# Performance work log

Hardware: AMD Instinct MI355X
Metric: run time of the kernel (lower is better)

Reference implementation:

```python
import jax, jax.numpy as jnp
import numpy as np

N_NODES = 100000
N_EDGES = 1600000
N_GRAPHS = 256
EPS = 1e-5  # GraphNorm / BatchNorm eps


def _seg_sum(x, seg, n):
    return jax.ops.segment_sum(x, seg, num_segments=n)


def setup_inputs() -> dict:
    key = jax.random.key(0)
    ks = jax.random.split(key, 24)
    f32 = jnp.float32

    def nrm(k, shape, s=0.05):
        return jax.random.normal(k, shape, f32) * s

    inp = {}
    inp["x"] = jax.random.normal(ks[0], (N_NODES, 64), f32)
    inp["edge_attr"] = jax.random.normal(ks[1], (N_EDGES, 8), f32)
    # edge_mlp: Linear(8,16) -> ReLU -> Linear(16,1); final bias +2 keeps degrees positive
    inp["em_w1"] = nrm(ks[2], (16, 8), 0.1); inp["em_b1"] = jnp.zeros((16,), f32)
    inp["em_w2"] = nrm(ks[3], (1, 16), 0.1); inp["em_b2"] = jnp.full((1,), 2.0, f32)
    # GCNConv weights stored (in, out); PyG GCNConv lin has no bias, separate bias after aggregation
    inp["conv_w0"] = nrm(ks[4], (64, 128)); inp["conv_b0"] = jnp.zeros((128,), f32)
    inp["conv_w1"] = nrm(ks[5], (128, 128)); inp["conv_b1"] = jnp.zeros((128,), f32)
    inp["conv_w2"] = nrm(ks[6], (128, 128)); inp["conv_b2"] = jnp.zeros((128,), f32)
    # GraphNorm params: weight=1, bias=0, mean_scale=1 (PyG init)
    for i in range(3):
        inp[f"gn_w{i}"] = jnp.ones((128,), f32)
        inp[f"gn_b{i}"] = jnp.zeros((128,), f32)
        inp[f"gn_ms{i}"] = jnp.ones((128,), f32)
    # MLP head (weights stored (in,out)); BatchNorm1d eval: running_mean=0, running_var=1
    inp["lin_w0"] = nrm(ks[7], (128, 256)); inp["lin_b0"] = jnp.zeros((256,), f32)
    inp["bn_g0"] = jnp.ones((256,), f32); inp["bn_b0"] = jnp.zeros((256,), f32)
    inp["lin_w1"] = nrm(ks[8], (256, 128)); inp["lin_b1"] = jnp.zeros((128,), f32)
    inp["bn_g1"] = jnp.ones((128,), f32); inp["bn_b1"] = jnp.zeros((128,), f32)
    inp["out_w"] = nrm(ks[9], (128, 1)); inp["out_b"] = jnp.zeros((1,), f32)
    inp["edge_index"] = jax.random.randint(ks[10], (2, N_EDGES), 0, N_NODES)
    inp["batch"] = jnp.sort(jax.random.randint(ks[11], (N_NODES,), 0, N_GRAPHS))
    return inp


def _gcn_conv(h, W, b, src, tgt, ew):
    # PyG GCNConv with edge_weight: add self-loops (weight 1), symmetric normalization
    hw = h @ W  # [N, out]
    deg = _seg_sum(ew, tgt, N_NODES) + 1.0  # in-degree incl. self-loop
    dinv = jnp.where(deg > 0, jax.lax.rsqrt(deg), 0.0)
    norm_e = dinv[src] * ew * dinv[tgt]  # [E]
    agg = _seg_sum(norm_e[:, None] * hw[src], tgt, N_NODES)
    agg = agg + (dinv * dinv)[:, None] * hw  # self-loop contribution
    return agg + b


def _graph_norm(h, batch, w, b, ms, cnt):
    mean = _seg_sum(h, batch, N_GRAPHS) / cnt[:, None]  # [G, C]
    sub = h - ms * mean[batch]
    var = _seg_sum(sub * sub, batch, N_GRAPHS) / cnt[:, None]
    return w * sub / jnp.sqrt(var + EPS)[batch] + b


def reference(x, edge_attr, em_w1, em_b1, em_w2, em_b2,
              conv_w0, conv_b0, conv_w1, conv_b1, conv_w2, conv_b2,
              gn_w0, gn_b0, gn_ms0, gn_w1, gn_b1, gn_ms1, gn_w2, gn_b2, gn_ms2,
              lin_w0, lin_b0, bn_g0, bn_b0, lin_w1, lin_b1, bn_g1, bn_b1,
              out_w, out_b, edge_index, batch):
    src, tgt = edge_index[0], edge_index[1]
    ew = (jax.nn.relu(edge_attr @ em_w1.T + em_b1) @ em_w2.T + em_b2).reshape(-1)  # [E]
    cnt = jnp.maximum(_seg_sum(jnp.ones((N_NODES,), x.dtype), batch, N_GRAPHS), 1.0)

    h = x
    layers = [(conv_w0, conv_b0, gn_w0, gn_b0, gn_ms0),
              (conv_w1, conv_b1, gn_w1, gn_b1, gn_ms1),
              (conv_w2, conv_b2, gn_w2, gn_b2, gn_ms2)]
    for W, b, gw, gb, gms in layers:
        h = _gcn_conv(h, W, b, src, tgt, ew)
        h = _graph_norm(h, batch, gw, gb, gms, cnt)
        h = jax.nn.relu(h)  # dropout is identity in eval mode

    pooled = _seg_sum(h, batch, N_GRAPHS) / cnt[:, None]  # global_mean_pool [G, 128]

    inv = 1.0 / jnp.sqrt(1.0 + EPS)  # BatchNorm1d eval: mean=0, var=1
    h = jax.nn.relu((pooled @ lin_w0 + lin_b0) * inv * bn_g0 + bn_b0)
    h = jax.nn.relu((h @ lin_w1 + lin_b1) * inv * bn_g1 + bn_b1)
    out = h @ out_w + out_b  # [G, 1]
    return (out, h)
```

## Files before the change

### kernel.cpp

```cpp
#include <hip/hip_runtime.h>

#define N_NODES 100000
#define N_EDGES 1600000
#define N_GRAPHS 256
#define EPS 1e-5f

#define SCAN_BLOCKS ((N_NODES + 255) / 256)

typedef __attribute__((ext_vector_type(8))) short bfrag8;
typedef __attribute__((ext_vector_type(4))) float facc4;

__device__ __forceinline__ void fma4(float4& a, float s, const float4& w) {
  a.x += s * w.x; a.y += s * w.y; a.z += s * w.z; a.w += s * w.w;
}

__device__ __forceinline__ unsigned short f2bf(float f) {
  union { float f; unsigned u; } x;
  x.f = f;
  unsigned r = x.u + 0x7FFF + ((x.u >> 16) & 1);
  return (unsigned short)(r >> 16);
}
__device__ __forceinline__ unsigned packbf(float a, float b) {
  return (unsigned)f2bf(a) | ((unsigned)f2bf(b) << 16);
}
__device__ __forceinline__ float4 bf4(uint2 v) {
  union { unsigned u; float f; } a, b, c, d;
  a.u = v.x << 16;
  b.u = v.x & 0xFFFF0000u;
  c.u = v.y << 16;
  d.u = v.y & 0xFFFF0000u;
  return make_float4(a.f, b.f, c.f, d.f);
}

__global__ __launch_bounds__(256) void k_edge_mlp(
    const float* __restrict__ ea, const float* __restrict__ w1,
    const float* __restrict__ b1, const float* __restrict__ w2,
    const float* __restrict__ b2, const int* __restrict__ tgt,
    float* __restrict__ ew, int* __restrict__ rowcnt,
    int* __restrict__ rank) {
  __shared__ float W1[128], B1[16], W2[16];
  int t = threadIdx.x;
  if (t < 128) W1[t] = w1[t];
  if (t < 16) { B1[t] = b1[t]; W2[t] = w2[t]; }
  __syncthreads();
  int e = blockIdx.x * 256 + t;
  if (e >= N_EDGES) return;
  const float4* ap = (const float4*)(ea + (size_t)e * 8);
  float4 a0 = ap[0], a1 = ap[1];
  float a[8] = {a0.x, a0.y, a0.z, a0.w, a1.x, a1.y, a1.z, a1.w};
  float out = b2[0];
#pragma unroll
  for (int i = 0; i < 16; ++i) {
    float h = B1[i];
#pragma unroll
    for (int j = 0; j < 8; ++j) h += a[j] * W1[i * 8 + j];
    out += fmaxf(h, 0.f) * W2[i];
  }
  ew[e] = out;
  rank[e] = atomicAdd(&rowcnt[tgt[e]], 1);
}

__global__ __launch_bounds__(256) void k_cvt(const float* __restrict__ x,
                                             unsigned* __restrict__ xb) {
  int i = blockIdx.x * 256 + threadIdx.x;
  if (i >= N_NODES * 64 / 8) return;
  const float4* p = (const float4*)(x + (size_t)i * 8);
  float4 a = p[0], b = p[1];
  uint4 o;
  o.x = packbf(a.x, a.y);
  o.y = packbf(a.z, a.w);
  o.z = packbf(b.x, b.y);
  o.w = packbf(b.z, b.w);
  ((uint4*)xb)[i] = o;
}

__global__ __launch_bounds__(256) void k_cvtw(
    const float* __restrict__ w1, const float* __restrict__ w2,
    unsigned short* __restrict__ o1, unsigned short* __restrict__ o2) {
  int id = blockIdx.x * 256 + threadIdx.x;
  const float* w = blockIdx.y ? w2 : w1;
  unsigned short* o = blockIdx.y ? o2 : o1;
  int n = id >> 7, k = id & 127;
  o[n * 128 + k] = f2bf(w[k * 128 + n]);
}

__global__ __launch_bounds__(256) void k_scan1(const int* __restrict__ cnt,
                                               int* __restrict__ bsum) {
  int i = blockIdx.x * 256 + threadIdx.x;
  int v = (i < N_NODES) ? cnt[i] : 0;
#pragma unroll
  for (int off = 32; off; off >>= 1) v += __shfl_down(v, off);
  __shared__ int ws[4];
  if ((threadIdx.x & 63) == 0) ws[threadIdx.x >> 6] = v;
  __syncthreads();
  if (threadIdx.x == 0) bsum[blockIdx.x] = ws[0] + ws[1] + ws[2] + ws[3];
}

__global__ __launch_bounds__(512) void k_scan2(const int* __restrict__ bsum,
                                               int* __restrict__ boff) {
  __shared__ int s[512];
  int t = threadIdx.x;
  s[t] = (t < SCAN_BLOCKS) ? bsum[t] : 0;
  __syncthreads();
  for (int off = 1; off < 512; off <<= 1) {
    int u = (t >= off) ? s[t - off] : 0;
    __syncthreads();
    s[t] += u;
    __syncthreads();
  }
  boff[t] = (t == 0) ? 0 : s[t - 1];
}

__global__ __launch_bounds__(256) void k_scan3(const int* __restrict__ cnt,
                                               const int* __restrict__ boff,
                                               int* __restrict__ rowstart) {
  __shared__ int s[256];
  int t = threadIdx.x;
  int i = blockIdx.x * 256 + t;
  int v = (i < N_NODES) ? cnt[i] : 0;
  s[t] = v;
  __syncthreads();
  for (int off = 1; off < 256; off <<= 1) {
    int u = (t >= off) ? s[t - off] : 0;
    __syncthreads();
    s[t] += u;
    __syncthreads();
  }
  if (i < N_NODES) {
    int pre = boff[blockIdx.x] + s[t] - v;
    rowstart[i] = pre;
    if (i == N_NODES - 1) rowstart[N_NODES] = pre + v;
  }
}

__global__ __launch_bounds__(256) void k_fill(
    const int* __restrict__ src, const int* __restrict__ tgt,
    const float* __restrict__ ew, const int* __restrict__ rank,
    const int* __restrict__ rowstart, int* __restrict__ src_s,
    float* __restrict__ ew_s) {
  int e = blockIdx.x * 256 + threadIdx.x;
  if (e >= N_EDGES) return;
  int p = rowstart[tgt[e]] + rank[e];
  src_s[p] = src[e];
  ew_s[p] = ew[e];
}

__global__ __launch_bounds__(256) void k_deg(const float* __restrict__ ew_s,
                                             const int* __restrict__ rowstart,
                                             float* __restrict__ dinv) {
  int n = blockIdx.x * 256 + threadIdx.x;
  if (n >= N_NODES) return;
  int rs = rowstart[n], re = rowstart[n + 1];
  float d = 1.f;
  for (int j = rs; j < re; ++j) d += ew_s[j];
  dinv[n] = d > 0.f ? rsqrtf(d) : 0.f;
}

__global__ __launch_bounds__(256) void k_scale(float* __restrict__ ew_s,
                                               const int* __restrict__ src_s,
                                               const int* __restrict__ rowstart,
                                               const float* __restrict__ dinv) {
  int n = blockIdx.x * 4 + (threadIdx.x >> 6);
  if (n >= N_NODES) return;
  int lane = threadIdx.x & 63;
  int rs = rowstart[n], re = rowstart[n + 1];
  float dv = dinv[n];
  for (int j = rs + lane; j < re; j += 64) ew_s[j] *= dinv[src_s[j]] * dv;
}

__global__ void k_starts(const int* __restrict__ batch, int* __restrict__ start) {
  int g = blockIdx.x * blockDim.x + threadIdx.x;
  if (g > N_GRAPHS) return;
  int lo = 0, hi = N_NODES;
  while (lo < hi) {
    int mid = (lo + hi) >> 1;
    if (batch[mid] < g) lo = mid + 1; else hi = mid;
  }
  start[g] = lo;
}

__global__ __launch_bounds__(256) void k_gather64b(
    const unsigned* __restrict__ xb, const float* __restrict__ ew_s,
    const int* __restrict__ src_s, const int* __restrict__ rowstart,
    const float* __restrict__ dinv, float* __restrict__ out) {
  const int t = threadIdx.x;
  const int n = blockIdx.x * 4 + (t >> 6);
  if (n >= N_NODES) return;
  const int lane = t & 63;
  const int q = lane >> 4;
  const int cl = lane & 15;
  const int rs = rowstart[n], re = rowstart[n + 1];
  const uint2* x2 = (const uint2*)xb;
  float4 a0 = make_float4(0.f, 0.f, 0.f, 0.f);
  float4 a1 = make_float4(0.f, 0.f, 0.f, 0.f);
  int j = rs;
  for (; j + 8 <= re; j += 8) {
    int i0 = j + q, i1 = j + 4 + q;
    float w0 = ew_s[i0], w1 = ew_s[i1];
    float4 v0 = bf4(x2[(size_t)src_s[i0] * 16 + cl]);
    float4 v1 = bf4(x2[(size_t)src_s[i1] * 16 + cl]);
    fma4(a0, w0, v0);
    fma4(a1, w1, v1);
  }
  for (; j + 4 <= re; j += 4) {
    int i0 = j + q;
    fma4(a0, ew_s[i0], bf4(x2[(size_t)src_s[i0] * 16 + cl]));
  }
  if (j + q < re) {
    fma4(a1, ew_s[j + q], bf4(x2[(size_t)src_s[j + q] * 16 + cl]));
  }
  a0.x += a1.x; a0.y += a1.y; a0.z += a1.z; a0.w += a1.w;
#pragma unroll
  for (int m = 16; m <= 32; m <<= 1) {
    a0.x += __shfl_xor(a0.x, m);
    a0.y += __shfl_xor(a0.y, m);
    a0.z += __shfl_xor(a0.z, m);
    a0.w += __shfl_xor(a0.w, m);
  }
  if (q == 0) {
    float dv = dinv[n];
    float4 hv = bf4(x2[(size_t)n * 16 + cl]);
    float4 r = make_float4(a0.x + dv * dv * hv.x, a0.y + dv * dv * hv.y,
                           a0.z + dv * dv * hv.z, a0.w + dv * dv * hv.w);
    ((float4*)out)[(size_t)n * 16 + cl] = r;
  }
}

template <int CIN>
__global__ __launch_bounds__(256) void k_hw0(
    const float* __restrict__ h, const float* __restrict__ W,
    const float* __restrict__ bias, float* __restrict__ hw) {
  constexpr int KT = 32;
  __shared__ float hs[64][36];
  __shared__ float Ws[KT][128];
  const int t = threadIdx.x;
  const int tn = t & 15, tc = t >> 4;
  const int base = blockIdx.x * 64;

  float acc[4][8];
#pragma unroll
  for (int i = 0; i < 4; ++i)
#pragma unroll
    for (int j = 0; j < 8; ++j) acc[i][j] = 0.f;

  const int ln = t >> 2;
  const int lk = (t & 3) * 8;
  const int wk = t >> 3;
  const int wc = (t & 7) * 16;

  for (int k0 = 0; k0 < CIN; k0 += KT) {
    __syncthreads();
    {
      int n = base + ln;
      float4 v0 = make_float4(0.f, 0.f, 0.f, 0.f), v1 = v0;
      if (n < N_NODES) {
        const float4* hp = (const float4*)(h + (size_t)n * CIN + k0 + lk);
        v0 = hp[0];
        v1 = hp[1];
      }
      *(float4*)&hs[ln][lk] = v0;
      *(float4*)&hs[ln][lk + 4] = v1;
      const float4* wp = (const float4*)(W + (size_t)(k0 + wk) * 128 + wc);
#pragma unroll
      for (int q = 0; q < 4; ++q) *(float4*)&Ws[wk][wc + q * 4] = wp[q];
    }
    __syncthreads();
#pragma unroll
    for (int kk = 0; kk < KT; kk += 4) {
      float4 hv[4];
#pragma unroll
      for (int i = 0; i < 4; ++i) hv[i] = *(const float4*)&hs[tn + 16 * i][kk];
#pragma unroll
      for (int dk = 0; dk < 4; ++dk) {
        float4 wa = *(const float4*)&Ws[kk + dk][tc * 4];
        float4 wb = *(const float4*)&Ws[kk + dk][64 + tc * 4];
#pragma unroll
        for (int i = 0; i < 4; ++i) {
          float hvv = (&hv[i].x)[dk];
          acc[i][0] += hvv * wa.x; acc[i][1] += hvv * wa.y;
          acc[i][2] += hvv * wa.z; acc[i][3] += hvv * wa.w;
          acc[i][4] += hvv * wb.x; acc[i][5] += hvv * wb.y;
          acc[i][6] += hvv * wb.z; acc[i][7] += hvv * wb.w;
        }
      }
    }
  }
  float4 b_lo = *(const float4*)&bias[tc * 4];
  float4 b_hi = *(const float4*)&bias[64 + tc * 4];
#pragma unroll
  for (int i = 0; i < 4; ++i) {
    int n = base + tn + 16 * i;
    if (n < N_NODES) {
      float* op = hw + (size_t)n * 128;
      *(float4*)&op[tc * 4] =
          make_float4(acc[i][0] + b_lo.x, acc[i][1] + b_lo.y,
                      acc[i][2] + b_lo.z, acc[i][3] + b_lo.w);
      *(float4*)&op[64 + tc * 4] =
          make_float4(acc[i][4] + b_hi.x, acc[i][5] + b_hi.y,
                      acc[i][6] + b_hi.z, acc[i][7] + b_hi.w);
    }
  }
}

__global__ __launch_bounds__(256) void k_hw_mfma(
    const float* __restrict__ h, const unsigned short* __restrict__ wt,
    const int* __restrict__ batch, const float* __restrict__ An,
    const float* __restrict__ Bn, unsigned short* __restrict__ hwb) {
  __shared__ unsigned short Asb[64][136];
  __shared__ unsigned short Wsb[128][136];
  const int t = threadIdx.x;
  const int base = blockIdx.x * 64;

  for (int i = t; i < 2048; i += 256) {
    int nr = i >> 4, k8 = (i & 15) * 8;
    *(uint4*)&Wsb[nr][k8] = *(const uint4*)&wt[nr * 128 + k8];
  }
  {
    const int ln = t >> 2;
    const int cg = (t & 3) * 32;
    const int n = base + ln;
    if (n < N_NODES) {
      const int g = batch[n];
      const float* hp = h + (size_t)n * 128;
      const float* Ap = An + (size_t)g * 128;
      const float* Bp = Bn + (size_t)g * 128;
#pragma unroll
      for (int c4 = 0; c4 < 8; ++c4) {
        int c = cg + c4 * 4;
        float4 v = *(const float4*)&hp[c];
        float4 Af = *(const float4*)&Ap[c];
        float4 Bf = *(const float4*)&Bp[c];
        uint2 o;
        o.x = packbf(fmaxf(Af.x * v.x + Bf.x, 0.f),
                     fmaxf(Af.y * v.y + Bf.y, 0.f));
        o.y = packbf(fmaxf(Af.z * v.z + Bf.z, 0.f),
                     fmaxf(Af.w * v.w + Bf.w, 0.f));
        *(uint2*)&Asb[ln][c] = o;
      }
    } else {
#pragma unroll
      for (int c4 = 0; c4 < 8; ++c4) {
        uint2 o;
        o.x = 0; o.y = 0;
        *(uint2*)&Asb[ln][cg + c4 * 4] = o;
      }
    }
  }
  __syncthreads();

  const int wv = t >> 6;
  const int lr = t & 15;
  const int lk = (t >> 4) & 3;
  const int m0 = wv * 16;

  bfrag8 af[4];
#pragma unroll
  for (int kc = 0; kc < 4; ++kc)
    af[kc] = *(const bfrag8*)&Asb[m0 + lr][kc * 32 + lk * 8];

#pragma unroll
  for (int nt = 0; nt < 8; ++nt) {
    facc4 c = {0.f, 0.f, 0.f, 0.f};
#pragma unroll
    for (int kc = 0; kc < 4; ++kc) {
      bfrag8 bf = *(const bfrag8*)&Wsb[nt * 16 + lr][kc * 32 + lk * 8];
      c = __builtin_amdgcn_mfma_f32_16x16x32_bf16(af[kc], bf, c, 0, 0, 0);
    }
    int col = nt * 16 + lr;
#pragma unroll
    for (int r = 0; r < 4; ++r) {
      int n = base + m0 + lk * 4 + r;
      if (n < N_NODES) hwb[(size_t)n * 128 + col] = f2bf(c[r]);
    }
  }
}

__global__ __launch_bounds__(256) void k_gatherb(
    const unsigned* __restrict__ hwb, const float* __restrict__ ew_s,
    const int* __restrict__ src_s, const int* __restrict__ rowstart,
    const float* __restrict__ dinv, const float* __restrict__ bias,
    float* __restrict__ agg) {
  const int t = threadIdx.x;
  const int n = blockIdx.x * 4 + (t >> 6);
  if (n >= N_NODES) return;
  const int lane = t & 63;
  const int q = lane >> 5;
  const int cl = lane & 31;
  const int rs = rowstart[n], re = rowstart[n + 1];
  const uint2* hb = (const uint2*)hwb;
  float4 a0 = make_float4(0.f, 0.f, 0.f, 0.f);
  float4 a1 = make_float4(0.f, 0.f, 0.f, 0.f);
  float4 a2 = make_float4(0.f, 0.f, 0.f, 0.f);
  float4 a3 = make_float4(0.f, 0.f, 0.f, 0.f);
  int j = rs;
  for (; j + 8 <= re; j += 8) {
    int i0 = j + q, i1 = j + 2 + q, i2 = j + 4 + q, i3 = j + 6 + q;
    float w0 = ew_s[i0], w1 = ew_s[i1], w2 = ew_s[i2], w3 = ew_s[i3];
    float4 v0 = bf4(hb[(size_t)src_s[i0] * 32 + cl]);
    float4 v1 = bf4(hb[(size_t)src_s[i1] * 32 + cl]);
    float4 v2 = bf4(hb[(size_t)src_s[i2] * 32 + cl]);
    float4 v3 = bf4(hb[(size_t)src_s[i3] * 32 + cl]);
    fma4(a0, w0, v0);
    fma4(a1, w1, v1);
    fma4(a2, w2, v2);
    fma4(a3, w3, v3);
  }
  for (; j + 2 <= re; j += 2) {
    int i0 = j + q;
    fma4(a0, ew_s[i0], bf4(hb[(size_t)src_s[i0] * 32 + cl]));
  }
  if (q == 0 && j < re) {
    fma4(a1, ew_s[j], bf4(hb[(size_t)src_s[j] * 32 + cl]));
  }
  a0.x += a1.x + a2.x + a3.x;
  a0.y += a1.y + a2.y + a3.y;
  a0.z += a1.z + a2.z + a3.z;
  a0.w += a1.w + a2.w + a3.w;
  a0.x += __shfl_xor(a0.x, 32);
  a0.y += __shfl_xor(a0.y, 32);
  a0.z += __shfl_xor(a0.z, 32);
  a0.w += __shfl_xor(a0.w, 32);
  if (q == 0) {
    float dv = dinv[n];
    float4 hv = bf4(hb[(size_t)n * 32 + cl]);
    float4 bv = ((const float4*)bias)[cl];
    float4 r = make_float4(a0.x + dv * dv * hv.x + bv.x,
                           a0.y + dv * dv * hv.y + bv.y,
                           a0.z + dv * dv * hv.z + bv.z,
                           a0.w + dv * dv * hv.w + bv.w);
    ((float4*)agg)[(size_t)n * 32 + cl] = r;
  }
}

__global__ __launch_bounds__(512) void k_gstats(
    const float* __restrict__ h, const int* __restrict__ start,
    const float* __restrict__ gw, const float* __restrict__ gb,
    const float* __restrict__ gms, float* __restrict__ An,
    float* __restrict__ Bn) {
  int g = blockIdx.x;
  int s = start[g], e = start[g + 1];
  int t = threadIdx.x, p = t >> 7, c = t & 127;
  float sum = 0.f, sq = 0.f;
  for (int n = s + p; n < e; n += 4) {
    float v = h[(size_t)n * 128 + c];
    sum += v;
    sq += v * v;
  }
  __shared__ float S[4][128], Q[4][128];
  S[p][c] = sum;
  Q[p][c] = sq;
  __syncthreads();
  if (t < 128) {
    float cnt = (float)max(e - s, 1);
    float mean = (S[0][t] + S[1][t] + S[2][t] + S[3][t]) / cnt;
    float e2 = (Q[0][t] + Q[1][t] + Q[2][t] + Q[3][t]) / cnt;
    float ms = gms[t];
    float var = fmaxf(e2 - ms * (2.f - ms) * mean * mean, 0.f);
    float scale = gw[t] / sqrtf(var + EPS);
    An[(size_t)g * 128 + t] = scale;
    Bn[(size_t)g * 128 + t] = gb[t] - scale * ms * mean;
  }
}

__global__ __launch_bounds__(512) void k_pool(
    const float* __restrict__ h, const int* __restrict__ start,
    const float* __restrict__ An, const float* __restrict__ Bn,
    float* __restrict__ pooled) {
  int g = blockIdx.x;
  int s = start[g], e = start[g + 1];
  int t = threadIdx.x, p = t >> 7, c = t & 127;
  float A = An[(size_t)g * 128 + c], B = Bn[(size_t)g * 128 + c];
  float sum = 0.f;
  for (int n = s + p; n < e; n += 4)
    sum += fmaxf(A * h[(size_t)n * 128 + c] + B, 0.f);
  __shared__ float S[4][128];
  S[p][c] = sum;
  __syncthreads();
  if (t < 128) {
    float cnt = (float)max(e - s, 1);
    pooled[g * 128 + t] = (S[0][t] + S[1][t] + S[2][t] + S[3][t]) / cnt;
  }
}

__global__ __launch_bounds__(256) void k_head(
    const float* __restrict__ pooled, const float* __restrict__ w0,
    const float* __restrict__ b0, const float* __restrict__ g0,
    const float* __restrict__ bb0, const float* __restrict__ w1,
    const float* __restrict__ b1, const float* __restrict__ g1,
    const float* __restrict__ bb1, const float* __restrict__ ow,
    const float* __restrict__ ob, float* __restrict__ out) {
  __shared__ float p[128], h1[256], h2[128];
  int g = blockIdx.x, t = threadIdx.x;
  const float inv = 1.0f / sqrtf(1.0f + EPS);
  if (t < 128) p[t] = pooled[g * 128 + t];
  __syncthreads();
  {
    float acc = b0[t];
#pragma unroll 8
    for (int k = 0; k < 128; ++k) acc += p[k] * w0[k * 256 + t];
    h1[t] = fmaxf(acc * inv * g0[t] + bb0[t], 0.f);
  }
  __syncthreads();
  if (t < 128) {
    float acc = b1[t];
#pragma unroll 8
    for (int k = 0; k < 256; ++k) acc += h1[k] * w1[k * 128 + t];
    float v = fmaxf(acc * inv * g1[t] + bb1[t], 0.f);
    h2[t] = v;
    out[N_GRAPHS + g * 128 + t] = v;
  }
  __syncthreads();
  if (t < 64) {
    float v = h2[t] * ow[t] + h2[t + 64] * ow[t + 64];
#pragma unroll
    for (int off = 32; off; off >>= 1) v += __shfl_down(v, off);
    if (t == 0) out[g] = v + ob[0];
  }
}

extern "C" void kernel_launch(void* const* d_in, const int* in_sizes, int n_in,
                              void* d_out, int out_size, void* d_ws,
                              size_t ws_size, hipStream_t stream) {
  const float* x = (const float*)d_in[0];
  const float* edge_attr = (const float*)d_in[1];
  const float* em_w1 = (const float*)d_in[2];
  const float* em_b1 = (const float*)d_in[3];
  const float* em_w2 = (const float*)d_in[4];
  const float* em_b2 = (const float*)d_in[5];
  const float* conv_w[3] = {(const float*)d_in[6], (const float*)d_in[8],
                            (const float*)d_in[10]};
  const float* conv_b[3] = {(const float*)d_in[7], (const float*)d_in[9],
                            (const float*)d_in[11]};
  const float* gn_w[3] = {(const float*)d_in[12], (const float*)d_in[15],
                          (const float*)d_in[18]};
  const float* gn_b[3] = {(const float*)d_in[13], (const float*)d_in[16],
                          (const float*)d_in[19]};
  const float* gn_ms[3] = {(const float*)d_in[14], (const float*)d_in[17],
                           (const float*)d_in[20]};
  const float* lin_w0 = (const float*)d_in[21];
  const float* lin_b0 = (const float*)d_in[22];
  const float* bn_g0 = (const float*)d_in[23];
  const float* bn_b0 = (const float*)d_in[24];
  const float* lin_w1 = (const float*)d_in[25];
  const float* lin_b1 = (const float*)d_in[26];
  const float* bn_g1 = (const float*)d_in[27];
  const float* bn_b1 = (const float*)d_in[28];
  const float* out_w = (const float*)d_in[29];
  const float* out_b = (const float*)d_in[30];
  const int* edge_index = (const int*)d_in[31];
  const int* batch = (const int*)d_in[32];
  const int* src = edge_index;
  const int* tgt = edge_index + N_EDGES;

  char* w = (char*)d_ws;
  size_t off = 0;
  auto carve = [&](size_t bytes) {
    void* p = w + off;
    off = (off + bytes + 511) & ~(size_t)511;
    return p;
  };
  float* ew = (float*)carve((size_t)N_EDGES * 4);
  int* rank = (int*)carve((size_t)N_EDGES * 4);
  float* dinv = (float*)carve((size_t)N_NODES * 4);
  int* rowcnt = (int*)carve((size_t)N_NODES * 4);
  int* rowstart = (int*)carve((size_t)(N_NODES + 1) * 4);
  int* bsum = (int*)carve((size_t)SCAN_BLOCKS * 4);
  int* boff = (int*)carve((size_t)512 * 4);
  int* src_s = (int*)carve((size_t)N_EDGES * 4);
  float* ew_s = (float*)carve((size_t)N_EDGES * 4);
  int* start = (int*)carve((N_GRAPHS + 1) * 4);
  float* AB = (float*)carve((size_t)6 * N_GRAPHS * 128 * 4);
  unsigned* xb = (unsigned*)carve((size_t)N_NODES * 64 * 2);
  unsigned* hwb = (unsigned*)carve((size_t)N_NODES * 128 * 2);
  unsigned short* wt1 = (unsigned short*)carve((size_t)128 * 128 * 2);
  unsigned short* wt2 = (unsigned short*)carve((size_t)128 * 128 * 2);
  float* big1 = (float*)carve((size_t)N_NODES * 128 * 4);
  float* big2 = (float*)carve((size_t)N_NODES * 128 * 4);
  float* pooled = (float*)carve((size_t)N_GRAPHS * 128 * 4);

  float* A0 = AB, *B0 = AB + N_GRAPHS * 128;
  float* A1 = AB + 2 * N_GRAPHS * 128, *B1 = AB + 3 * N_GRAPHS * 128;
  float* A2 = AB + 4 * N_GRAPHS * 128, *B2 = AB + 5 * N_GRAPHS * 128;

  hipMemsetAsync(rowcnt, 0, (size_t)N_NODES * 4, stream);

  k_edge_mlp<<<(N_EDGES + 255) / 256, 256, 0, stream>>>(
      edge_attr, em_w1, em_b1, em_w2, em_b2, tgt, ew, rowcnt, rank);
  k_cvt<<<(N_NODES * 64 / 8 + 255) / 256, 256, 0, stream>>>(x, xb);
  k_cvtw<<<dim3(64, 2), 256, 0, stream>>>(conv_w[1], conv_w[2], wt1, wt2);
  k_scan1<<<SCAN_BLOCKS, 256, 0, stream>>>(rowcnt, bsum);
  k_scan2<<<1, 512, 0, stream>>>(bsum, boff);
  k_scan3<<<SCAN_BLOCKS, 256, 0, stream>>>(rowcnt, boff, rowstart);
  k_fill<<<(N_EDGES + 255) / 256, 256, 0, stream>>>(src, tgt, ew, rank,
                                                    rowstart, src_s, ew_s);
  k_deg<<<(N_NODES + 255) / 256, 256, 0, stream>>>(ew_s, rowstart, dinv);
  k_scale<<<(N_NODES + 3) / 4, 256, 0, stream>>>(ew_s, src_s, rowstart, dinv);
  k_starts<<<1, 512, 0, stream>>>(batch, start);

  const int ggrid = (N_NODES + 3) / 4;
  const int hwgrid = (N_NODES + 63) / 64;

  k_gather64b<<<ggrid, 256, 0, stream>>>(xb, ew_s, src_s, rowstart, dinv,
                                         big2);
  k_hw0<64><<<hwgrid, 256, 0, stream>>>(big2, conv_w[0], conv_b[0], big1);
  k_gstats<<<N_GRAPHS, 512, 0, stream>>>(big1, start, gn_w[0], gn_b[0],
                                         gn_ms[0], A0, B0);
  k_hw_mfma<<<hwgrid, 256, 0, stream>>>(big1, wt1, batch, A0, B0,
                                        (unsigned short*)hwb);
  k_gatherb<<<ggrid, 256, 0, stream>>>(hwb, ew_s, src_s, rowstart, dinv,
                                       conv_b[1], big2);
  k_gstats<<<N_GRAPHS, 512, 0, stream>>>(big2, start, gn_w[1], gn_b[1],
                                         gn_ms[1], A1, B1);
  k_hw_mfma<<<hwgrid, 256, 0, stream>>>(big2, wt2, batch, A1, B1,
                                        (unsigned short*)hwb);
  k_gatherb<<<ggrid, 256, 0, stream>>>(hwb, ew_s, src_s, rowstart, dinv,
                                       conv_b[2], big1);
  k_gstats<<<N_GRAPHS, 512, 0, stream>>>(big1, start, gn_w[2], gn_b[2],
                                         gn_ms[2], A2, B2);

  k_pool<<<N_GRAPHS, 512, 0, stream>>>(big1, start, A2, B2, pooled);
  k_head<<<N_GRAPHS, 256, 0, stream>>>(pooled, lin_w0, lin_b0, bn_g0, bn_b0,
                                       lin_w1, lin_b1, bn_g1, bn_b1, out_w,
                                       out_b, (float*)d_out);
}
```

Before: 594.2 us.

## Store intermediates in bf16, pack edge metadata, use MFMA for first layer

Interleaves source index and edge weight into a single uint2 metadata array so each gather reads one 8-byte record instead of two separate arrays. All node-level intermediates (aggregated features, layer outputs) are now stored as bf16 instead of fp32, halving the traffic of the gstats, pool and hw kernels. The first-layer FP32 tiled GEMM is replaced by a bf16 MFMA kernel with pre-transposed bf16 weights. This cuts memory bandwidth but adds bf16 rounding at more points, which may affect accuracy.

```diff
diff --git a/kernel.cpp b/kernel.cpp
--- a/kernel.cpp
+++ b/kernel.cpp
@@ -23,13 +23,19 @@
 __device__ __forceinline__ unsigned packbf(float a, float b) {
   return (unsigned)f2bf(a) | ((unsigned)f2bf(b) << 16);
 }
-__device__ __forceinline__ float4 bf4(uint2 v) {
+__device__ __forceinline__ float4 bf4(unsigned lo, unsigned hi) {
   union { unsigned u; float f; } a, b, c, d;
-  a.u = v.x << 16;
-  b.u = v.x & 0xFFFF0000u;
-  c.u = v.y << 16;
-  d.u = v.y & 0xFFFF0000u;
+  a.u = lo << 16;
+  b.u = lo & 0xFFFF0000u;
+  c.u = hi << 16;
+  d.u = hi & 0xFFFF0000u;
   return make_float4(a.f, b.f, c.f, d.f);
+}
+__device__ __forceinline__ float bfat(const unsigned* tb, int idx) {
+  unsigned u = tb[idx >> 1];
+  union { unsigned u; float f; } v;
+  v.u = (idx & 1) ? (u & 0xFFFF0000u) : (u << 16);
+  return v.f;
 }
 
 __global__ __launch_bounds__(256) void k_edge_mlp(
@@ -84,6 +90,14 @@
   o[n * 128 + k] = f2bf(w[k * 128 + n]);
 }
 
+__global__ __launch_bounds__(256) void k_cvtw0(const float* __restrict__ w0,
+                                               unsigned short* __restrict__ o) {
+  int id = blockIdx.x * 256 + threadIdx.x;
+  if (id >= 8192) return;
+  int n = id >> 6, k = id & 63;
+  o[n * 64 + k] = f2bf(w0[k * 128 + n]);
+}
+
 __global__ __launch_bounds__(256) void k_scan1(const int* __restrict__ cnt,
                                                int* __restrict__ bsum) {
   int i = blockIdx.x * 256 + threadIdx.x;
@@ -136,28 +150,31 @@
 __global__ __launch_bounds__(256) void k_fill(
     const int* __restrict__ src, const int* __restrict__ tgt,
     const float* __restrict__ ew, const int* __restrict__ rank,
-    const int* __restrict__ rowstart, int* __restrict__ src_s,
-    float* __restrict__ ew_s) {
+    const int* __restrict__ rowstart, uint2* __restrict__ meta) {
   int e = blockIdx.x * 256 + threadIdx.x;
   if (e >= N_EDGES) return;
   int p = rowstart[tgt[e]] + rank[e];
-  src_s[p] = src[e];
-  ew_s[p] = ew[e];
-}
-
-__global__ __launch_bounds__(256) void k_deg(const float* __restrict__ ew_s,
+  union { float f; unsigned u; } w;
+  w.f = ew[e];
+  meta[p] = make_uint2(w.u, (unsigned)src[e]);
+}
+
+__global__ __launch_bounds__(256) void k_deg(const uint2* __restrict__ meta,
                                              const int* __restrict__ rowstart,
                                              float* __restrict__ dinv) {
   int n = blockIdx.x * 256 + threadIdx.x;
   if (n >= N_NODES) return;
   int rs = rowstart[n], re = rowstart[n + 1];
   float d = 1.f;
-  for (int j = rs; j < re; ++j) d += ew_s[j];
+  for (int j = rs; j < re; ++j) {
+    union { unsigned u; float f; } w;
+    w.u = meta[j].x;
+    d += w.f;
+  }
   dinv[n] = d > 0.f ? rsqrtf(d) : 0.f;
 }
 
-__global__ __launch_bounds__(256) void k_scale(float* __restrict__ ew_s,
-                                               const int* __restrict__ src_s,
+__global__ __launch_bounds__(256) void k_scale(uint2* __restrict__ meta,
                                                const int* __restrict__ rowstart,
                                                const float* __restrict__ dinv) {
   int n = blockIdx.x * 4 + (threadIdx.x >> 6);
@@ -165,7 +182,13 @@
   int lane = threadIdx.x & 63;
   int rs = rowstart[n], re = rowstart[n + 1];
   float dv = dinv[n];
-  for (int j = rs + lane; j < re; j += 64) ew_s[j] *= dinv[src_s[j]] * dv;
+  for (int j = rs + lane; j < re; j += 64) {
+    uint2 m = meta[j];
+    union { unsigned u; float f; } w;
+    w.u = m.x;
+    w.f *= dinv[m.y] * dv;
+    meta[j].x = w.u;
+  }
 }
 
 __global__ void k_starts(const int* __restrict__ batch, int* __restrict__ start) {
@@ -180,9 +203,9 @@
 }
 
 __global__ __launch_bounds__(256) void k_gather64b(
-    const unsigned* __restrict__ xb, const float* __restrict__ ew_s,
-    const int* __restrict__ src_s, const int* __restrict__ rowstart,
-    const float* __restrict__ dinv, float* __restrict__ out) {
+    const unsigned* __restrict__ xb, const uint2* __restrict__ meta,
+    const int* __restrict__ rowstart, const float* __restrict__ dinv,
+    unsigned* __restrict__ aggxb) {
   const int t = threadIdx.x;
   const int n = blockIdx.x * 4 + (t >> 6);
   if (n >= N_NODES) return;
@@ -195,19 +218,27 @@
   float4 a1 = make_float4(0.f, 0.f, 0.f, 0.f);
   int j = rs;
   for (; j + 8 <= re; j += 8) {
-    int i0 = j + q, i1 = j + 4 + q;
-    float w0 = ew_s[i0], w1 = ew_s[i1];
-    float4 v0 = bf4(x2[(size_t)src_s[i0] * 16 + cl]);
-    float4 v1 = bf4(x2[(size_t)src_s[i1] * 16 + cl]);
-    fma4(a0, w0, v0);
-    fma4(a1, w1, v1);
+    uint2 m0 = meta[j + q], m1 = meta[j + 4 + q];
+    union { unsigned u; float f; } w0, w1;
+    w0.u = m0.x; w1.u = m1.x;
+    uint2 v0 = x2[(size_t)m0.y * 16 + cl];
+    uint2 v1 = x2[(size_t)m1.y * 16 + cl];
+    fma4(a0, w0.f, bf4(v0.x, v0.y));
+    fma4(a1, w1.f, bf4(v1.x, v1.y));
   }
   for (; j + 4 <= re; j += 4) {
-    int i0 = j + q;
-    fma4(a0, ew_s[i0], bf4(x2[(size_t)src_s[i0] * 16 + cl]));
+    uint2 m0 = meta[j + q];
+    union { unsigned u; float f; } w0;
+    w0.u = m0.x;
+    uint2 v0 = x2[(size_t)m0.y * 16 + cl];
+    fma4(a0, w0.f, bf4(v0.x, v0.y));
   }
   if (j + q < re) {
-    fma4(a1, ew_s[j + q], bf4(x2[(size_t)src_s[j + q] * 16 + cl]));
+    uint2 m0 = meta[j + q];
+    union { unsigned u; float f; } w0;
+    w0.u = m0.x;
+    uint2 v0 = x2[(size_t)m0.y * 16 + cl];
+    fma4(a1, w0.f, bf4(v0.x, v0.y));
   }
   a0.x += a1.x; a0.y += a1.y; a0.z += a1.z; a0.w += a1.w;
 #pragma unroll
@@ -219,91 +250,73 @@
   }
   if (q == 0) {
     float dv = dinv[n];
-    float4 hv = bf4(x2[(size_t)n * 16 + cl]);
-    float4 r = make_float4(a0.x + dv * dv * hv.x, a0.y + dv * dv * hv.y,
-                           a0.z + dv * dv * hv.z, a0.w + dv * dv * hv.w);
-    ((float4*)out)[(size_t)n * 16 + cl] = r;
-  }
-}
-
-template <int CIN>
-__global__ __launch_bounds__(256) void k_hw0(
-    const float* __restrict__ h, const float* __restrict__ W,
-    const float* __restrict__ bias, float* __restrict__ hw) {
-  constexpr int KT = 32;
-  __shared__ float hs[64][36];
-  __shared__ float Ws[KT][128];
+    uint2 hvb = x2[(size_t)n * 16 + cl];
+    float4 hv = bf4(hvb.x, hvb.y);
+    uint2 o;
+    o.x = packbf(a0.x + dv * dv * hv.x, a0.y + dv * dv * hv.y);
+    o.y = packbf(a0.z + dv * dv * hv.z, a0.w + dv * dv * hv.w);
+    *(uint2*)&aggxb[(size_t)n * 32 + cl * 2] = o;
+  }
+}
+
+__global__ __launch_bounds__(256) void k_hw_mfma0(
+    const unsigned short* __restrict__ aggxb,
+    const unsigned short* __restrict__ wt0, const float* __restrict__ bias,
+    unsigned short* __restrict__ h1b) {
+  __shared__ unsigned short Asb[64][72];
+  __shared__ unsigned short Wsb[128][72];
   const int t = threadIdx.x;
-  const int tn = t & 15, tc = t >> 4;
   const int base = blockIdx.x * 64;
 
-  float acc[4][8];
-#pragma unroll
-  for (int i = 0; i < 4; ++i)
-#pragma unroll
-    for (int j = 0; j < 8; ++j) acc[i][j] = 0.f;
-
-  const int ln = t >> 2;
-  const int lk = (t & 3) * 8;
-  const int wk = t >> 3;
-  const int wc = (t & 7) * 16;
-
-  for (int k0 = 0; k0 < CIN; k0 += KT) {
-    __syncthreads();
-    {
-      int n = base + ln;
-      float4 v0 = make_float4(0.f, 0.f, 0.f, 0.f), v1 = v0;
-      if (n < N_NODES) {
-        const float4* hp = (const float4*)(h + (size_t)n * CIN + k0 + lk);
-        v0 = hp[0];
-        v1 = hp[1];
-      }
-      *(float4*)&hs[ln][lk] = v0;
-      *(float4*)&hs[ln][lk + 4] = v1;
-      const float4* wp = (const float4*)(W + (size_t)(k0 + wk) * 128 + wc);
-#pragma unroll
-      for (int q = 0; q < 4; ++q) *(float4*)&Ws[wk][wc + q * 4] = wp[q];
+  for (int i = t; i < 1024; i += 256) {
+    int nr = i >> 3, k8 = (i & 7) * 8;
+    *(uint4*)&Wsb[nr][k8] = *(const uint4*)&wt0[nr * 64 + k8];
+  }
+  {
+    const int ln = t >> 2;
+    const int kp = (t & 3) * 16;
+    const int n = base + ln;
+    if (n < N_NODES) {
+      *(uint4*)&Asb[ln][kp] = *(const uint4*)&aggxb[(size_t)n * 64 + kp];
+      *(uint4*)&Asb[ln][kp + 8] = *(const uint4*)&aggxb[(size_t)n * 64 + kp + 8];
+    } else {
+      uint4 z = make_uint4(0, 0, 0, 0);
+      *(uint4*)&Asb[ln][kp] = z;
+      *(uint4*)&Asb[ln][kp + 8] = z;
     }
-    __syncthreads();
-#pragma unroll
-    for (int kk = 0; kk < KT; kk += 4) {
-      float4 hv[4];
-#pragma unroll
-      for (int i = 0; i < 4; ++i) hv[i] = *(const float4*)&hs[tn + 16 * i][kk];
-#pragma unroll
-      for (int dk = 0; dk < 4; ++dk) {
-        float4 wa = *(const float4*)&Ws[kk + dk][tc * 4];
-        float4 wb = *(const float4*)&Ws[kk + dk][64 + tc * 4];
-#pragma unroll
-        for (int i = 0; i < 4; ++i) {
-          float hvv = (&hv[i].x)[dk];
-          acc[i][0] += hvv * wa.x; acc[i][1] += hvv * wa.y;
-          acc[i][2] += hvv * wa.z; acc[i][3] += hvv * wa.w;
-          acc[i][4] += hvv * wb.x; acc[i][5] += hvv * wb.y;
-          acc[i][6] += hvv * wb.z; acc[i][7] += hvv * wb.w;
-        }
-      }
+  }
+  __syncthreads();
+
+  const int wv = t >> 6;
+  const int lr = t & 15;
+  const int lk = (t >> 4) & 3;
+  const int m0 = wv * 16;
+
+  bfrag8 af[2];
+#pragma unroll
+  for (int kc = 0; kc < 2; ++kc)
+    af[kc] = *(const bfrag8*)&Asb[m0 + lr][kc * 32 + lk * 8];
+
+#pragma unroll
+  for (int nt = 0; nt < 8; ++nt) {
+    facc4 c = {0.f, 0.f, 0.f, 0.f};
+#pragma unroll
+    for (int kc = 0; kc < 2; ++kc) {
+      bfrag8 bf = *(const bfrag8*)&Wsb[nt * 16 + lr][kc * 32 + lk * 8];
+      c = __builtin_amdgcn_mfma_f32_16x16x32_bf16(af[kc], bf, c, 0, 0, 0);
     }
-  }
-  float4 b_lo = *(const float4*)&bias[tc * 4];
-  float4 b_hi = *(const float4*)&bias[64 + tc * 4];
-#pragma unroll
-  for (int i = 0; i < 4; ++i) {
-    int n = base + tn + 16 * i;
-    if (n < N_NODES) {
-      float* op = hw + (size_t)n * 128;
-      *(float4*)&op[tc * 4] =
-          make_float4(acc[i][0] + b_lo.x, acc[i][1] + b_lo.y,
-                      acc[i][2] + b_lo.z, acc[i][3] + b_lo.w);
-      *(float4*)&op[64 + tc * 4] =
-          make_float4(acc[i][4] + b_hi.x, acc[i][5] + b_hi.y,
-                      acc[i][6] + b_hi.z, acc[i][7] + b_hi.w);
+    int col = nt * 16 + lr;
+    float bv = bias[col];
+#pragma unroll
+    for (int r = 0; r < 4; ++r) {
+      int n = base + m0 + lk * 4 + r;
+      if (n < N_NODES) h1b[(size_t)n * 128 + col] = f2bf(c[r] + bv);
     }
   }
 }
 
 __global__ __launch_bounds__(256) void k_hw_mfma(
-    const float* __restrict__ h, const unsigned short* __restrict__ wt,
+    const unsigned* __restrict__ hb, const unsigned short* __restrict__ wt,
     const int* __restrict__ batch, const float* __restrict__ An,
     const float* __restrict__ Bn, unsigned short* __restrict__ hwb) {
   __shared__ unsigned short Asb[64][136];
@@ -321,29 +334,32 @@
     const int n = base + ln;
     if (n < N_NODES) {
       const int g = batch[n];
-      const float* hp = h + (size_t)n * 128;
+      const uint4* hp = (const uint4*)(hb + (size_t)n * 64);
       const float* Ap = An + (size_t)g * 128;
       const float* Bp = Bn + (size_t)g * 128;
 #pragma unroll
-      for (int c4 = 0; c4 < 8; ++c4) {
-        int c = cg + c4 * 4;
-        float4 v = *(const float4*)&hp[c];
-        float4 Af = *(const float4*)&Ap[c];
-        float4 Bf = *(const float4*)&Bp[c];
-        uint2 o;
-        o.x = packbf(fmaxf(Af.x * v.x + Bf.x, 0.f),
-                     fmaxf(Af.y * v.y + Bf.y, 0.f));
-        o.y = packbf(fmaxf(Af.z * v.z + Bf.z, 0.f),
-                     fmaxf(Af.w * v.w + Bf.w, 0.f));
-        *(uint2*)&Asb[ln][c] = o;
+      for (int qq = 0; qq < 4; ++qq) {
+        int c = cg + qq * 8;
+        uint4 v = hp[(t & 3) * 4 + qq];
+        float4 lo = bf4(v.x, v.y);
+        float4 hi = bf4(v.z, v.w);
+        float4 Alo = *(const float4*)&Ap[c], Blo = *(const float4*)&Bp[c];
+        float4 Ahi = *(const float4*)&Ap[c + 4], Bhi = *(const float4*)&Bp[c + 4];
+        uint4 o;
+        o.x = packbf(fmaxf(Alo.x * lo.x + Blo.x, 0.f),
+                     fmaxf(Alo.y * lo.y + Blo.y, 0.f));
+        o.y = packbf(fmaxf(Alo.z * lo.z + Blo.z, 0.f),
+                     fmaxf(Alo.w * lo.w + Blo.w, 0.f));
+        o.z = packbf(fmaxf(Ahi.x * hi.x + Bhi.x, 0.f),
+                     fmaxf(Ahi.y * hi.y + Bhi.y, 0.f));
+        o.w = packbf(fmaxf(Ahi.z * hi.z + Bhi.z, 0.f),
+                     fmaxf(Ahi.w * hi.w + Bhi.w, 0.f));
+        *(uint4*)&Asb[ln][c] = o;
       }
     } else {
-#pragma unroll
-      for (int c4 = 0; c4 < 8; ++c4) {
-        uint2 o;
-        o.x = 0; o.y = 0;
-        *(uint2*)&Asb[ln][cg + c4 * 4] = o;
-      }
+      uint4 z = make_uint4(0, 0, 0, 0);
+#pragma unroll
+      for (int qq = 0; qq < 4; ++qq) *(uint4*)&Asb[ln][cg + qq * 8] = z;
     }
   }
   __syncthreads();
@@ -376,10 +392,9 @@
 }
 
 __global__ __launch_bounds__(256) void k_gatherb(
-    const unsigned* __restrict__ hwb, const float* __restrict__ ew_s,
-    const int* __restrict__ src_s, const int* __restrict__ rowstart,
-    const float* __restrict__ dinv, const float* __restrict__ bias,
-    float* __restrict__ agg) {
+    const unsigned* __restrict__ hwb, const uint2* __restrict__ meta,
+    const int* __restrict__ rowstart, const float* __restrict__ dinv,
+    const float* __restrict__ bias, unsigned* __restrict__ aggb) {
   const int t = threadIdx.x;
   const int n = blockIdx.x * 4 + (t >> 6);
   if (n >= N_NODES) return;
@@ -394,23 +409,32 @@
   float4 a3 = make_float4(0.f, 0.f, 0.f, 0.f);
   int j = rs;
   for (; j + 8 <= re; j += 8) {
-    int i0 = j + q, i1 = j + 2 + q, i2 = j + 4 + q, i3 = j + 6 + q;
-    float w0 = ew_s[i0], w1 = ew_s[i1], w2 = ew_s[i2], w3 = ew_s[i3];
-    float4 v0 = bf4(hb[(size_t)src_s[i0] * 32 + cl]);
-    float4 v1 = bf4(hb[(size_t)src_s[i1] * 32 + cl]);
-    float4 v2 = bf4(hb[(size_t)src_s[i2] * 32 + cl]);
-    float4 v3 = bf4(hb[(size_t)src_s[i3] * 32 + cl]);
-    fma4(a0, w0, v0);
-    fma4(a1, w1, v1);
-    fma4(a2, w2, v2);
-    fma4(a3, w3, v3);
+    uint2 m0 = meta[j + q], m1 = meta[j + 2 + q];
+    uint2 m2 = meta[j + 4 + q], m3 = meta[j + 6 + q];
+    union { unsigned u; float f; } w0, w1, w2, w3;
+    w0.u = m0.x; w1.u = m1.x; w2.u = m2.x; w3.u = m3.x;
+    uint2 v0 = hb[(size_t)m0.y * 32 + cl];
+    uint2 v1 = hb[(size_t)m1.y * 32 + cl];
+    uint2 v2 = hb[(size_t)m2.y * 32 + cl];
+    uint2 v3 = hb[(size_t)m3.y * 32 + cl];
+    fma4(a0, w0.f, bf4(v0.x, v0.y));
+    fma4(a1, w1.f, bf4(v1.x, v1.y));
+    fma4(a2, w2.f, bf4(v2.x, v2.y));
+    fma4(a3, w3.f, bf4(v3.x, v3.y));
   }
   for (; j + 2 <= re; j += 2) {
-    int i0 = j + q;
-    fma4(a0, ew_s[i0], bf4(hb[(size_t)src_s[i0] * 32 + cl]));
+    uint2 m0 = meta[j + q];
+    union { unsigned u; float f; } w0;
+    w0.u = m0.x;
+    uint2 v0 = hb[(size_t)m0.y * 32 + cl];
+    fma4(a0, w0.f, bf4(v0.x, v0.y));
   }
   if (q == 0 && j < re) {
-    fma4(a1, ew_s[j], bf4(hb[(size_t)src_s[j] * 32 + cl]));
+    uint2 m0 = meta[j];
+    union { unsigned u; float f; } w0;
+    w0.u = m0.x;
+    uint2 v0 = hb[(size_t)m0.y * 32 + cl];
+    fma4(a1, w0.f, bf4(v0.x, v0.y));
   }
   a0.x += a1.x + a2.x + a3.x;
   a0.y += a1.y + a2.y + a3.y;
@@ -422,18 +446,18 @@
   a0.w += __shfl_xor(a0.w, 32);
   if (q == 0) {
     float dv = dinv[n];
-    float4 hv = bf4(hb[(size_t)n * 32 + cl]);
+    uint2 hvb = hb[(size_t)n * 32 + cl];
+    float4 hv = bf4(hvb.x, hvb.y);
     float4 bv = ((const float4*)bias)[cl];
-    float4 r = make_float4(a0.x + dv * dv * hv.x + bv.x,
-                           a0.y + dv * dv * hv.y + bv.y,
-                           a0.z + dv * dv * hv.z + bv.z,
-                           a0.w + dv * dv * hv.w + bv.w);
-    ((float4*)agg)[(size_t)n * 32 + cl] = r;
+    uint2 o;
+    o.x = packbf(a0.x + dv * dv * hv.x + bv.x, a0.y + dv * dv * hv.y + bv.y);
+    o.y = packbf(a0.z + dv * dv * hv.z + bv.z, a0.w + dv * dv * hv.w + bv.w);
+    *(uint2*)&aggb[(size_t)n * 64 + cl * 2] = o;
   }
 }
 
 __global__ __launch_bounds__(512) void k_gstats(
-    const float* __restrict__ h, const int* __restrict__ start,
+    const unsigned* __restrict__ hb, const int* __restrict__ start,
     const float* __restrict__ gw, const float* __restrict__ gb,
     const float* __restrict__ gms, float* __restrict__ An,
     float* __restrict__ Bn) {
@@ -442,7 +466,7 @@
   int t = threadIdx.x, p = t >> 7, c = t & 127;
   float sum = 0.f, sq = 0.f;
   for (int n = s + p; n < e; n += 4) {
-    float v = h[(size_t)n * 128 + c];
+    float v = bfat(hb + (size_t)n * 64, c);
     sum += v;
     sq += v * v;
   }
@@ -463,7 +487,7 @@
 }
 
 __global__ __launch_bounds__(512) void k_pool(
-    const float* __restrict__ h, const int* __restrict__ start,
+    const unsigned* __restrict__ hb, const int* __restrict__ start,
     const float* __restrict__ An, const float* __restrict__ Bn,
     float* __restrict__ pooled) {
   int g = blockIdx.x;
@@ -472,7 +496,7 @@
   float A = An[(size_t)g * 128 + c], B = Bn[(size_t)g * 128 + c];
   float sum = 0.f;
   for (int n = s + p; n < e; n += 4)
-    sum += fmaxf(A * h[(size_t)n * 128 + c] + B, 0.f);
+    sum += fmaxf(A * bfat(hb + (size_t)n * 64, c) + B, 0.f);
   __shared__ float S[4][128];
   S[p][c] = sum;
   __syncthreads();
@@ -566,16 +590,18 @@
   int* rowstart = (int*)carve((size_t)(N_NODES + 1) * 4);
   int* bsum = (int*)carve((size_t)SCAN_BLOCKS * 4);
   int* boff = (int*)carve((size_t)512 * 4);
-  int* src_s = (int*)carve((size_t)N_EDGES * 4);
-  float* ew_s = (float*)carve((size_t)N_EDGES * 4);
+  uint2* meta = (uint2*)carve((size_t)N_EDGES * 8);
   int* start = (int*)carve((N_GRAPHS + 1) * 4);
   float* AB = (float*)carve((size_t)6 * N_GRAPHS * 128 * 4);
   unsigned* xb = (unsigned*)carve((size_t)N_NODES * 64 * 2);
+  unsigned* aggxb = (unsigned*)carve((size_t)N_NODES * 64 * 2);
+  unsigned* h1b = (unsigned*)carve((size_t)N_NODES * 128 * 2);
   unsigned* hwb = (unsigned*)carve((size_t)N_NODES * 128 * 2);
+  unsigned* agg1b = (unsigned*)carve((size_t)N_NODES * 128 * 2);
+  unsigned* agg2b = (unsigned*)carve((size_t)N_NODES * 128 * 2);
+  unsigned short* wt0 = (unsigned short*)carve((size_t)128 * 64 * 2);
   unsigned short* wt1 = (unsigned short*)carve((size_t)128 * 128 * 2);
   unsigned short* wt2 = (unsigned short*)carve((size_t)128 * 128 * 2);
-  float* big1 = (float*)carve((size_t)N_NODES * 128 * 4);
-  float* big2 = (float*)carve((size_t)N_NODES * 128 * 4);
   float* pooled = (float*)carve((size_t)N_GRAPHS * 128 * 4);
 
   float* A0 = AB, *B0 = AB + N_GRAPHS * 128;
@@ -588,37 +614,38 @@
       edge_attr, em_w1, em_b1, em_w2, em_b2, tgt, ew, rowcnt, rank);
   k_cvt<<<(N_NODES * 64 / 8 + 255) / 256, 256, 0, stream>>>(x, xb);
   k_cvtw<<<dim3(64, 2), 256, 0, stream>>>(conv_w[1], conv_w[2], wt1, wt2);
+  k_cvtw0<<<32, 256, 0, stream>>>(conv_w[0], wt0);
   k_scan1<<<SCAN_BLOCKS, 256, 0, stream>>>(rowcnt, bsum);
   k_scan2<<<1, 512, 0, stream>>>(bsum, boff);
   k_scan3<<<SCAN_BLOCKS, 256, 0, stream>>>(rowcnt, boff, rowstart);
   k_fill<<<(N_EDGES + 255) / 256, 256, 0, stream>>>(src, tgt, ew, rank,
-                                                    rowstart, src_s, ew_s);
-  k_deg<<<(N_NODES + 255) / 256, 256, 0, stream>>>(ew_s, rowstart, dinv);
-  k_scale<<<(N_NODES + 3) / 4, 256, 0, stream>>>(ew_s, src_s, rowstart, dinv);
+                                                    rowstart, meta);
+  k_deg<<<(N_NODES + 255) / 256, 256, 0, stream>>>(meta, rowstart, dinv);
+  k_scale<<<(N_NODES + 3) / 4, 256, 0, stream>>>(meta, rowstart, dinv);
   k_starts<<<1, 512, 0, stream>>>(batch, start);
 
   const int ggrid = (N_NODES + 3) / 4;
   const int hwgrid = (N_NODES + 63) / 64;
 
-  k_gather64b<<<ggrid, 256, 0, stream>>>(xb, ew_s, src_s, rowstart, dinv,
-                                         big2);
-  k_hw0<64><<<hwgrid, 256, 0, stream>>>(big2, conv_w[0], conv_b[0], big1);
-  k_gstats<<<N_GRAPHS, 512, 0, stream>>>(big1, start, gn_w[0], gn_b[0],
+  k_gather64b<<<ggrid, 256, 0, stream>>>(xb, meta, rowstart, dinv, aggxb);
+  k_hw_mfma0<<<hwgrid, 256, 0, stream>>>((unsigned short*)aggxb, wt0,
+                                         conv_b[0], (unsigned short*)h1b);
+  k_gstats<<<N_GRAPHS, 512, 0, stream>>>(h1b, start, gn_w[0], gn_b[0],
                                          gn_ms[0], A0, B0);
-  k_hw_mfma<<<hwgrid, 256, 0, stream>>>(big1, wt1, batch, A0, B0,
+  k_hw_mfma<<<hwgrid, 256, 0, stream>>>(h1b, wt1, batch, A0, B0,
                                         (unsigned short*)hwb);
-  k_gatherb<<<ggrid, 256, 0, stream>>>(hwb, ew_s, src_s, rowstart, dinv,
-                                       conv_b[1], big2);
-  k_gstats<<<N_GRAPHS, 512, 0, stream>>>(big2, start, gn_w[1], gn_b[1],
+  k_gatherb<<<ggrid, 256, 0, stream>>>(hwb, meta, rowstart, dinv, conv_b[1],
+                                       agg1b);
+  k_gstats<<<N_GRAPHS, 512, 0, stream>>>(agg1b, start, gn_w[1], gn_b[1],
                                          gn_ms[1], A1, B1);
-  k_hw_mfma<<<hwgrid, 256, 0, stream>>>(big2, wt2, batch, A1, B1,
+  k_hw_mfma<<<hwgrid, 256, 0, stream>>>(agg1b, wt2, batch, A1, B1,
                                         (unsigned short*)hwb);
-  k_gatherb<<<ggrid, 256, 0, stream>>>(hwb, ew_s, src_s, rowstart, dinv,
-                                       conv_b[2], big1);
-  k_gstats<<<N_GRAPHS, 512, 0, stream>>>(big1, start, gn_w[2], gn_b[2],
+  k_gatherb<<<ggrid, 256, 0, stream>>>(hwb, meta, rowstart, dinv, conv_b[2],
+                                       agg2b);
+  k_gstats<<<N_GRAPHS, 512, 0, stream>>>(agg2b, start, gn_w[2], gn_b[2],
                                          gn_ms[2], A2, B2);
 
-  k_pool<<<N_GRAPHS, 512, 0, stream>>>(big1, start, A2, B2, pooled);
+  k_pool<<<N_GRAPHS, 512, 0, stream>>>(agg2b, start, A2, B2, pooled);
   k_head<<<N_GRAPHS, 256, 0, stream>>>(pooled, lin_w0, lin_b0, bn_g0, bn_b0,
                                        lin_w1, lin_b1, bn_g1, bn_b1, out_w,
                                        out_b, (float*)d_out);
```

New measurement: 531.0 us. 1.12x faster.
